# Kernel tuning notes

Hardware: AMD Instinct MI355X
Metric: run time of the kernel (lower is better)

Reference implementation:

```python
import jax, jax.numpy as jnp
import numpy as np

NUM_CIRCLES = 7
B, D_IN, D_HID, D_OUT = 4096, 2048, 3584, 2048  # D_HID % 7 == 0 (7 * 512)


def setup_inputs() -> dict:
    key = jax.random.key(0)
    k1, k2, k3, k4 = jax.random.split(key, 4)
    x = jax.random.normal(k1, (B, D_IN), dtype=jnp.float32)
    # FlowerOfLife: 7 bias-free Linear(D_IN -> D_HID//7) weights, stacked [7, D_HID//7, D_IN]
    W_flower = jax.random.normal(k2, (NUM_CIRCLES, D_HID // NUM_CIRCLES, D_IN), dtype=jnp.float32) / np.sqrt(D_IN).astype(np.float32)
    # Merkaba: two bias-free Linear(D_HID -> D_OUT)
    W_male = jax.random.normal(k3, (D_OUT, D_HID), dtype=jnp.float32) / np.sqrt(D_HID).astype(np.float32)
    W_female = jax.random.normal(k4, (D_OUT, D_HID), dtype=jnp.float32) / np.sqrt(D_HID).astype(np.float32)
    return {"x": x, "W_flower": W_flower, "W_male": W_male, "W_female": W_female}


def reference(x, W_flower, W_male, W_female):
    # --- VesicaPiscisOperation: sacred overlap with the batch-rolled neighbor ---
    x2 = jnp.roll(x, 1, axis=0)
    dist = jnp.linalg.norm(x - x2, axis=1, keepdims=True)          # [B, 1]
    overlap = jax.nn.relu(1.0 - jnp.abs(dist - 1.0))               # [B, 1]
    x_overlap = x * (1.0 + overlap)                                # per-row scaling

    # --- FlowerOfLifeProjection: 7 parallel projections, phase-shift first 2 dims ---
    circ = jnp.einsum('bd,cod->bco', x_overlap, W_flower)          # [B, 7, D_HID//7]
    phases = 2.0 * jnp.pi * jnp.arange(NUM_CIRCLES, dtype=jnp.float32) / NUM_CIRCLES
    phase_shift = jnp.stack([jnp.cos(phases), jnp.sin(phases)], axis=-1)  # [7, 2]
    circ = circ.at[:, :, :2].multiply(phase_shift[None, :, :])
    x_expanded = circ.reshape(x.shape[0], -1)                      # [B, D_HID]

    # --- MerkabaRotation: counter-rotating transforms + sigmoid phase lock ---
    male = x_expanded @ W_male.T                                   # [B, D_OUT]
    female = x_expanded[:, ::-1] @ W_female.T                      # flip(-1) then Linear
    phase_lock = jax.nn.sigmoid(jnp.sum(male * female, axis=-1, keepdims=True))
    return phase_lock * male + (1.0 - phase_lock) * female
```

## Files before the change

kernel.cpp:

```cpp
#include <hip/hip_runtime.h>
#include <hip/hip_bf16.h>
#include <math.h>

#define B_DIM 4096
#define D_IN  2048
#define D_HID 3584
#define D_OUT 2048

typedef __bf16 bf16;
typedef float  floatx4 __attribute__((ext_vector_type(4)));
typedef bf16   bf16x8  __attribute__((ext_vector_type(8)));
typedef bf16   bf16x4  __attribute__((ext_vector_type(4)));

typedef __attribute__((address_space(1))) const void* gptr1;
typedef __attribute__((address_space(3))) void*       lptr3;

__device__ __forceinline__ void load_lds16(const void* g, void* l) {
    __builtin_amdgcn_global_load_lds((gptr1)g, (lptr3)l, 16, 0, 0);
}

struct HL { bf16 h, l; };
__device__ __forceinline__ HL split2(float v) {
    HL r;
    r.h = (bf16)v;
    r.l = (bf16)(v - (float)r.h);
    return r;
}

__global__ __launch_bounds__(256) void vesica_kernel(const float* __restrict__ x,
                                                     bf16* __restrict__ xh,
                                                     bf16* __restrict__ xl) {
    const int b  = blockIdx.x;
    const int bp = (b == 0) ? (B_DIM - 1) : (b - 1);
    const int t  = threadIdx.x;

    const floatx4* xr = (const floatx4*)(x + (size_t)b  * D_IN);
    const floatx4* pr = (const floatx4*)(x + (size_t)bp * D_IN);
    const floatx4 v0 = xr[t * 2], v1 = xr[t * 2 + 1];
    const floatx4 p0 = pr[t * 2], p1 = pr[t * 2 + 1];

    float s = 0.f;
#pragma unroll
    for (int j = 0; j < 4; ++j) {
        const float d0 = v0[j] - p0[j], d1 = v1[j] - p1[j];
        s += d0 * d0 + d1 * d1;
    }
#pragma unroll
    for (int off = 32; off > 0; off >>= 1) s += __shfl_down(s, off, 64);

    __shared__ float red[4];
    const int wave = t >> 6, lane = t & 63;
    if (lane == 0) red[wave] = s;
    __syncthreads();
    const float dist = sqrtf(red[0] + red[1] + red[2] + red[3]);
    const float sc   = 1.f + fmaxf(0.f, 1.f - fabsf(dist - 1.f));

    bf16x8 h, l;
#pragma unroll
    for (int j = 0; j < 4; ++j) {
        const HL a  = split2(v0[j] * sc);
        const HL b2 = split2(v1[j] * sc);
        h[j] = a.h;      l[j] = a.l;
        h[4 + j] = b2.h; l[4 + j] = b2.l;
    }
    ((bf16x8*)(xh + (size_t)b * D_IN))[t] = h;
    ((bf16x8*)(xl + (size_t)b * D_IN))[t] = l;
}

__global__ __launch_bounds__(256) void split_kernel(const float* __restrict__ w,
                                                    bf16* __restrict__ wh,
                                                    bf16* __restrict__ wl) {
    const size_t i = (size_t)blockIdx.x * 256 + threadIdx.x;
    const floatx4 a = ((const floatx4*)w)[i * 2];
    const floatx4 b = ((const floatx4*)w)[i * 2 + 1];
    bf16x8 h, l;
#pragma unroll
    for (int j = 0; j < 4; ++j) {
        const HL u = split2(a[j]);
        const HL v = split2(b[j]);
        h[j] = u.h;     l[j] = u.l;
        h[4 + j] = v.h; l[4 + j] = v.l;
    }
    ((bf16x8*)wh)[i] = h;
    ((bf16x8*)wl)[i] = l;
}

__global__ __launch_bounds__(256) void flipsplit_kernel(const float* __restrict__ w,
                                                        bf16* __restrict__ wh,
                                                        bf16* __restrict__ wl) {
    const int i = blockIdx.x * 256 + threadIdx.x;
    const int o = i / 448;
    const int g = i - o * 448;
    const float* src = w + (size_t)o * 3584 + (size_t)(447 - g) * 8;
    const floatx4 a = ((const floatx4*)src)[0];
    const floatx4 b = ((const floatx4*)src)[1];
    bf16x8 h, l;
#pragma unroll
    for (int j = 0; j < 4; ++j) {
        const HL u = split2(b[3 - j]);
        const HL v = split2(a[3 - j]);
        h[j] = u.h;     l[j] = u.l;
        h[4 + j] = v.h; l[4 + j] = v.l;
    }
    ((bf16x8*)wh)[(size_t)o * 448 + g] = h;
    ((bf16x8*)wl)[(size_t)o * 448 + g] = l;
}

__global__ __launch_bounds__(256) void tsplit_kernel(const float* __restrict__ w,
                                                     bf16* __restrict__ th,
                                                     bf16* __restrict__ tl) {
    __shared__ float tile[64][65];
    const int d0 = blockIdx.x * 64;
    const int h0 = blockIdx.y * 64;
    const int t  = threadIdx.x;
    const int r  = t >> 4;
    const int cg = (t & 15) << 2;

#pragma unroll
    for (int i = 0; i < 4; ++i) {
        const int hr = r + i * 16;
        const floatx4 v = *(const floatx4*)&w[(size_t)(h0 + hr) * 2048 + d0 + cg];
        tile[hr][cg]     = v[0];
        tile[hr][cg + 1] = v[1];
        tile[hr][cg + 2] = v[2];
        tile[hr][cg + 3] = v[3];
    }
    __syncthreads();

    float pm[4];
#pragma unroll
    for (int j = 0; j < 4; ++j) {
        const int h  = h0 + cg + j;
        const int hm = h & 511;
        float p = 1.f;
        if (hm < 2) {
            const float ph = 0.8975979010256552f * (float)(h >> 9);
            p = (hm == 0) ? cosf(ph) : sinf(ph);
        }
        pm[j] = p;
    }

#pragma unroll
    for (int i = 0; i < 4; ++i) {
        const int dr = r + i * 16;
        bf16x4 hh, ll;
#pragma unroll
        for (int j = 0; j < 4; ++j) {
            const HL u = split2(tile[cg + j][dr] * pm[j]);
            hh[j] = u.h;
            ll[j] = u.l;
        }
        const size_t o = (size_t)(d0 + dr) * 3584 + h0 + cg;
        *(bf16x4*)&th[o] = hh;
        *(bf16x4*)&tl[o] = ll;
    }
}

__global__ __launch_bounds__(512, 2) void gemm3_single(const bf16* __restrict__ Ah,
                                                       const bf16* __restrict__ Al,
                                                       const bf16* __restrict__ Bh,
                                                       const bf16* __restrict__ Bl,
                                                       bf16* __restrict__ C0,
                                                       bf16* __restrict__ C1,
                                                       int M, int N, int K) {
    __shared__ bf16 sAh[2][8192], sAl[2][8192];
    __shared__ bf16 sBh[2][4096], sBl[2][4096];

    const int tid  = threadIdx.x;
    const int wave = tid >> 6;
    const int lane = tid & 63;
    const int m0   = blockIdx.y * 256;
    const int n0   = blockIdx.x * 128;
    const int wm   = wave >> 1;
    const int wn   = wave & 1;

    floatx4 acc[4][4];
#pragma unroll
    for (int i = 0; i < 4; ++i)
#pragma unroll
        for (int j = 0; j < 4; ++j) acc[i][j] = (floatx4){0.f, 0.f, 0.f, 0.f};

    const int lr  = lane & 15;
    const int cq  = lane >> 4;
    const int hsw = (lr >> 1) & 7;

    auto stage = [&](int kt, int bsel) {
#pragma unroll
        for (int i = 0; i < 2; ++i) {
            const int q = (i << 9) + tid;
            const int p = q ^ ((q >> 3) & 7);
            const int r = p >> 2, c = p & 3;
            const size_t ga = (size_t)(m0 + r) * K + kt + c * 8;
            load_lds16(&Ah[ga], &sAh[bsel][q << 3]);
            load_lds16(&Al[ga], &sAl[bsel][q << 3]);
        }
        {
            const int q = tid;
            const int p = q ^ ((q >> 3) & 7);
            const int r = p >> 2, c = p & 3;
            const size_t gb = (size_t)(n0 + r) * K + kt + c * 8;
            load_lds16(&Bh[gb], &sBh[bsel][q << 3]);
            load_lds16(&Bl[gb], &sBl[bsel][q << 3]);
        }
    };

    stage(0, 0);
    __syncthreads();

    int buf = 0;
    for (int kt = 0; kt < K; kt += 32) {
        if (kt + 32 < K) stage(kt + 32, buf ^ 1);

        bf16x8 ahf[4], alf[4], bhf[4], blf[4];
#pragma unroll
        for (int mi = 0; mi < 4; ++mi) {
            const int row = wm * 64 + mi * 16 + lr;
            const int off = (((row << 2) + cq) ^ hsw) << 3;
            ahf[mi] = *(const bf16x8*)&sAh[buf][off];
            alf[mi] = *(const bf16x8*)&sAl[buf][off];
        }
#pragma unroll
        for (int ni = 0; ni < 4; ++ni) {
            const int row = wn * 64 + ni * 16 + lr;
            const int off = (((row << 2) + cq) ^ hsw) << 3;
            bhf[ni] = *(const bf16x8*)&sBh[buf][off];
            blf[ni] = *(const bf16x8*)&sBl[buf][off];
        }

#pragma unroll
        for (int mi = 0; mi < 4; ++mi)
#pragma unroll
            for (int ni = 0; ni < 4; ++ni) {
                acc[mi][ni] = __builtin_amdgcn_mfma_f32_16x16x32_bf16(
                    ahf[mi], bhf[ni], acc[mi][ni], 0, 0, 0);
                acc[mi][ni] = __builtin_amdgcn_mfma_f32_16x16x32_bf16(
                    alf[mi], bhf[ni], acc[mi][ni], 0, 0, 0);
                acc[mi][ni] = __builtin_amdgcn_mfma_f32_16x16x32_bf16(
                    ahf[mi], blf[ni], acc[mi][ni], 0, 0, 0);
            }

        __syncthreads();
        buf ^= 1;
    }

    const int rq = (lane >> 4) << 2;
    const int cl = lane & 15;
#pragma unroll
    for (int mi = 0; mi < 4; ++mi) {
#pragma unroll
        for (int ni = 0; ni < 4; ++ni) {
            const int col = n0 + wn * 64 + ni * 16 + cl;
#pragma unroll
            for (int r = 0; r < 4; ++r) {
                const int row = m0 + wm * 64 + mi * 16 + rq + r;
                const size_t idx = (size_t)row * N + col;
                const HL u = split2(acc[mi][ni][r]);
                C0[idx] = u.h;
                C1[idx] = u.l;
            }
        }
    }
}

__global__ __launch_bounds__(512, 2) void gemm3_dual(const bf16* __restrict__ Ah,
                                                     const bf16* __restrict__ Al,
                                                     const bf16* __restrict__ Bmh,
                                                     const bf16* __restrict__ Bml,
                                                     const bf16* __restrict__ Bfh,
                                                     const bf16* __restrict__ Bfl,
                                                     float* __restrict__ Cm,
                                                     float* __restrict__ Cf,
                                                     int M, int N, int K) {
    __shared__ bf16 sAh[2][8192], sAl[2][8192];
    __shared__ bf16 sMh[2][4096], sMl[2][4096];
    __shared__ bf16 sFh[2][4096], sFl[2][4096];

    const int tid  = threadIdx.x;
    const int wave = tid >> 6;
    const int lane = tid & 63;
    const int m0   = blockIdx.y * 256;
    const int n0   = blockIdx.x * 128;
    const int wm   = wave >> 1;
    const int wn   = wave & 1;

    floatx4 am[4][4], af[4][4];
#pragma unroll
    for (int i = 0; i < 4; ++i)
#pragma unroll
        for (int j = 0; j < 4; ++j) {
            am[i][j] = (floatx4){0.f, 0.f, 0.f, 0.f};
            af[i][j] = (floatx4){0.f, 0.f, 0.f, 0.f};
        }

    const int lr  = lane & 15;
    const int cq  = lane >> 4;
    const int hsw = (lr >> 1) & 7;

    auto stage = [&](int kt, int bsel) {
#pragma unroll
        for (int i = 0; i < 2; ++i) {
            const int q = (i << 9) + tid;
            const int p = q ^ ((q >> 3) & 7);
            const int r = p >> 2, c = p & 3;
            const size_t ga = (size_t)(m0 + r) * K + kt + c * 8;
            load_lds16(&Ah[ga], &sAh[bsel][q << 3]);
            load_lds16(&Al[ga], &sAl[bsel][q << 3]);
        }
        {
            const int q = tid;
            const int p = q ^ ((q >> 3) & 7);
            const int r = p >> 2, c = p & 3;
            const size_t gb = (size_t)(n0 + r) * K + kt + c * 8;
            load_lds16(&Bmh[gb], &sMh[bsel][q << 3]);
            load_lds16(&Bml[gb], &sMl[bsel][q << 3]);
            load_lds16(&Bfh[gb], &sFh[bsel][q << 3]);
            load_lds16(&Bfl[gb], &sFl[bsel][q << 3]);
        }
    };

    stage(0, 0);
    __syncthreads();

    int buf = 0;
    for (int kt = 0; kt < K; kt += 32) {
        if (kt + 32 < K) stage(kt + 32, buf ^ 1);

        bf16x8 ahf[4], alf[4];
#pragma unroll
        for (int mi = 0; mi < 4; ++mi) {
            const int row = wm * 64 + mi * 16 + lr;
            const int off = (((row << 2) + cq) ^ hsw) << 3;
            ahf[mi] = *(const bf16x8*)&sAh[buf][off];
            alf[mi] = *(const bf16x8*)&sAl[buf][off];
        }
#pragma unroll
        for (int ni = 0; ni < 4; ++ni) {
            const int row = wn * 64 + ni * 16 + lr;
            const int off = (((row << 2) + cq) ^ hsw) << 3;
            const bf16x8 mh = *(const bf16x8*)&sMh[buf][off];
            const bf16x8 ml = *(const bf16x8*)&sMl[buf][off];
            const bf16x8 fh = *(const bf16x8*)&sFh[buf][off];
            const bf16x8 fl = *(const bf16x8*)&sFl[buf][off];
#pragma unroll
            for (int mi = 0; mi < 4; ++mi) {
                am[mi][ni] = __builtin_amdgcn_mfma_f32_16x16x32_bf16(
                    ahf[mi], mh, am[mi][ni], 0, 0, 0);
                am[mi][ni] = __builtin_amdgcn_mfma_f32_16x16x32_bf16(
                    alf[mi], mh, am[mi][ni], 0, 0, 0);
                am[mi][ni] = __builtin_amdgcn_mfma_f32_16x16x32_bf16(
                    ahf[mi], ml, am[mi][ni], 0, 0, 0);
                af[mi][ni] = __builtin_amdgcn_mfma_f32_16x16x32_bf16(
                    ahf[mi], fh, af[mi][ni], 0, 0, 0);
                af[mi][ni] = __builtin_amdgcn_mfma_f32_16x16x32_bf16(
                    alf[mi], fh, af[mi][ni], 0, 0, 0);
                af[mi][ni] = __builtin_amdgcn_mfma_f32_16x16x32_bf16(
                    ahf[mi], fl, af[mi][ni], 0, 0, 0);
            }
        }

        __syncthreads();
        buf ^= 1;
    }

    const int rq = (lane >> 4) << 2;
    const int cl = lane & 15;
#pragma unroll
    for (int mi = 0; mi < 4; ++mi) {
#pragma unroll
        for (int ni = 0; ni < 4; ++ni) {
            const int col = n0 + wn * 64 + ni * 16 + cl;
#pragma unroll
            for (int r = 0; r < 4; ++r) {
                const int row = m0 + wm * 64 + mi * 16 + rq + r;
                const size_t idx = (size_t)row * N + col;
                Cm[idx] = am[mi][ni][r];
                Cf[idx] = af[mi][ni][r];
            }
        }
    }
}

__global__ __launch_bounds__(256) void combine_kernel(const float* __restrict__ male,
                                                      const float* __restrict__ female,
                                                      float* __restrict__ out) {
    const int b = blockIdx.x;
    const int t = threadIdx.x;

    const floatx4* m4 = (const floatx4*)(male   + (size_t)b * D_OUT);
    const floatx4* f4 = (const floatx4*)(female + (size_t)b * D_OUT);
    const floatx4 mv0 = m4[t * 2], mv1 = m4[t * 2 + 1];
    const floatx4 fv0 = f4[t * 2], fv1 = f4[t * 2 + 1];

    float s = 0.f;
#pragma unroll
    for (int j = 0; j < 4; ++j) s += mv0[j] * fv0[j] + mv1[j] * fv1[j];
#pragma unroll
    for (int off = 32; off > 0; off >>= 1) s += __shfl_down(s, off, 64);

    __shared__ float red[4];
    const int wave = t >> 6, lane = t & 63;
    if (lane == 0) red[wave] = s;
    __syncthreads();
    const float dot = red[0] + red[1] + red[2] + red[3];
    const float pl  = 1.f / (1.f + expf(-dot));

    floatx4 o0, o1;
#pragma unroll
    for (int j = 0; j < 4; ++j) {
        o0[j] = pl * mv0[j] + (1.f - pl) * fv0[j];
        o1[j] = pl * mv1[j] + (1.f - pl) * fv1[j];
    }
    floatx4* o4 = (floatx4*)(out + (size_t)b * D_OUT);
    o4[t * 2]     = o0;
    o4[t * 2 + 1] = o1;
}

extern "C" void kernel_launch(void* const* d_in, const int* in_sizes, int n_in,
                              void* d_out, int out_size, void* d_ws, size_t ws_size,
                              hipStream_t stream) {
    const float* x   = (const float*)d_in[0];
    const float* Wfl = (const float*)d_in[1];
    const float* Wm  = (const float*)d_in[2];
    const float* Wfe = (const float*)d_in[3];
    float* out = (float*)d_out;
    (void)in_sizes; (void)n_in; (void)out_size; (void)ws_size;

    char* ws = (char*)d_ws;
    bf16*  xo_hi   = (bf16*)(ws);
    bf16*  xo_lo   = (bf16*)(ws + 16777216);
    bf16*  Wc_hi   = (bf16*)(ws + 33554432);
    bf16*  Wc_lo   = (bf16*)(ws + 50331648);
    bf16*  WflT_hi = (bf16*)(ws + 67108864);
    bf16*  WflT_lo = (bf16*)(ws + 81788928);
    bf16*  Wcat_hi = (bf16*)(ws + 96468992);
    bf16*  Wcat_lo = (bf16*)(ws + 125829120);
    float* male    = (float*)(ws + 67108864);
    float* female  = (float*)(ws + 100663296);

    vesica_kernel<<<B_DIM, 256, 0, stream>>>(x, xo_hi, xo_lo);

    tsplit_kernel<<<dim3(D_IN / 64, D_HID / 64), 256, 0, stream>>>(Wfl, WflT_hi, WflT_lo);

    split_kernel<<<(D_OUT * D_HID / 8) / 256, 256, 0, stream>>>(Wm, Wcat_hi, Wcat_lo);
    flipsplit_kernel<<<(D_OUT * (D_HID / 8)) / 256, 256, 0, stream>>>(
        Wfe, Wcat_hi + (size_t)D_OUT * D_HID, Wcat_lo + (size_t)D_OUT * D_HID);

    gemm3_single<<<dim3(D_IN / 128, (2 * D_OUT) / 256), 512, 0, stream>>>(
        Wcat_hi, Wcat_lo, WflT_hi, WflT_lo, Wc_hi, Wc_lo,
        2 * D_OUT, D_IN, D_HID);

    gemm3_dual<<<dim3(D_OUT / 128, B_DIM / 256), 512, 0, stream>>>(
        xo_hi, xo_lo,
        Wc_hi, Wc_lo,
        Wc_hi + (size_t)D_OUT * D_IN, Wc_lo + (size_t)D_OUT * D_IN,
        male, female, B_DIM, D_OUT, D_IN);

    combine_kernel<<<B_DIM, 256, 0, stream>>>(male, female, out);
}
```

Baseline: 547.4 us.

## Unify GEMMs into 128x128 templated kernel and split dual GEMM into two launches

Replaces the 256x128-tile single and dual GEMM kernels with one templated 128x128-tile, 256-thread kernel that writes either bf16 hi/lo splits or fp32 output. The dual male/female GEMM becomes two separate launches that each re-read the activation operand. The smaller tile lowers LDS and register use and increases the block count. In exchange, each block reuses less data per tile, the x operand is loaded twice from global memory, and one more kernel is launched.

```diff
diff --git a/kernel.cpp b/kernel.cpp
--- a/kernel.cpp
+++ b/kernel.cpp
@@ -156,23 +156,24 @@
     }
 }
 
-__global__ __launch_bounds__(512, 2) void gemm3_single(const bf16* __restrict__ Ah,
-                                                       const bf16* __restrict__ Al,
-                                                       const bf16* __restrict__ Bh,
-                                                       const bf16* __restrict__ Bl,
-                                                       bf16* __restrict__ C0,
-                                                       bf16* __restrict__ C1,
-                                                       int M, int N, int K) {
-    __shared__ bf16 sAh[2][8192], sAl[2][8192];
+template<int BF16OUT>
+__global__ __launch_bounds__(256, 2) void gemm3_db(const bf16* __restrict__ Ah,
+                                                   const bf16* __restrict__ Al,
+                                                   const bf16* __restrict__ Bh,
+                                                   const bf16* __restrict__ Bl,
+                                                   void* __restrict__ C0p,
+                                                   void* __restrict__ C1p,
+                                                   int M, int N, int K) {
+    __shared__ bf16 sAh[2][4096], sAl[2][4096];
     __shared__ bf16 sBh[2][4096], sBl[2][4096];
 
     const int tid  = threadIdx.x;
     const int wave = tid >> 6;
     const int lane = tid & 63;
-    const int m0   = blockIdx.y * 256;
+    const int m0   = blockIdx.y * 128;
     const int n0   = blockIdx.x * 128;
-    const int wm   = wave >> 1;
-    const int wn   = wave & 1;
+    const int wm   = wave & 1;
+    const int wn   = wave >> 1;
 
     floatx4 acc[4][4];
 #pragma unroll
@@ -187,18 +188,13 @@
     auto stage = [&](int kt, int bsel) {
 #pragma unroll
         for (int i = 0; i < 2; ++i) {
-            const int q = (i << 9) + tid;
+            const int q = (i << 8) + tid;
             const int p = q ^ ((q >> 3) & 7);
             const int r = p >> 2, c = p & 3;
             const size_t ga = (size_t)(m0 + r) * K + kt + c * 8;
+            const size_t gb = (size_t)(n0 + r) * K + kt + c * 8;
             load_lds16(&Ah[ga], &sAh[bsel][q << 3]);
             load_lds16(&Al[ga], &sAl[bsel][q << 3]);
-        }
-        {
-            const int q = tid;
-            const int p = q ^ ((q >> 3) & 7);
-            const int r = p >> 2, c = p & 3;
-            const size_t gb = (size_t)(n0 + r) * K + kt + c * 8;
             load_lds16(&Bh[gb], &sBh[bsel][q << 3]);
             load_lds16(&Bl[gb], &sBl[bsel][q << 3]);
         }
@@ -211,7 +207,7 @@
     for (int kt = 0; kt < K; kt += 32) {
         if (kt + 32 < K) stage(kt + 32, buf ^ 1);
 
-        bf16x8 ahf[4], alf[4], bhf[4], blf[4];
+        bf16x8 ahf[4], alf[4];
 #pragma unroll
         for (int mi = 0; mi < 4; ++mi) {
             const int row = wm * 64 + mi * 16 + lr;
@@ -223,21 +219,18 @@
         for (int ni = 0; ni < 4; ++ni) {
             const int row = wn * 64 + ni * 16 + lr;
             const int off = (((row << 2) + cq) ^ hsw) << 3;
-            bhf[ni] = *(const bf16x8*)&sBh[buf][off];
-            blf[ni] = *(const bf16x8*)&sBl[buf][off];
-        }
-
-#pragma unroll
-        for (int mi = 0; mi < 4; ++mi)
-#pragma unroll
-            for (int ni = 0; ni < 4; ++ni) {
+            const bf16x8 bh = *(const bf16x8*)&sBh[buf][off];
+            const bf16x8 bl = *(const bf16x8*)&sBl[buf][off];
+#pragma unroll
+            for (int mi = 0; mi < 4; ++mi) {
                 acc[mi][ni] = __builtin_amdgcn_mfma_f32_16x16x32_bf16(
-                    ahf[mi], bhf[ni], acc[mi][ni], 0, 0, 0);
+                    ahf[mi], bh, acc[mi][ni], 0, 0, 0);
                 acc[mi][ni] = __builtin_amdgcn_mfma_f32_16x16x32_bf16(
-                    alf[mi], bhf[ni], acc[mi][ni], 0, 0, 0);
+                    alf[mi], bh, acc[mi][ni], 0, 0, 0);
                 acc[mi][ni] = __builtin_amdgcn_mfma_f32_16x16x32_bf16(
-                    ahf[mi], blf[ni], acc[mi][ni], 0, 0, 0);
+                    ahf[mi], bl, acc[mi][ni], 0, 0, 0);
             }
+        }
 
         __syncthreads();
         buf ^= 1;
@@ -254,127 +247,13 @@
             for (int r = 0; r < 4; ++r) {
                 const int row = m0 + wm * 64 + mi * 16 + rq + r;
                 const size_t idx = (size_t)row * N + col;
-                const HL u = split2(acc[mi][ni][r]);
-                C0[idx] = u.h;
-                C1[idx] = u.l;
-            }
-        }
-    }
-}
-
-__global__ __launch_bounds__(512, 2) void gemm3_dual(const bf16* __restrict__ Ah,
-                                                     const bf16* __restrict__ Al,
-                                                     const bf16* __restrict__ Bmh,
-                                                     const bf16* __restrict__ Bml,
-                                                     const bf16* __restrict__ Bfh,
-                                                     const bf16* __restrict__ Bfl,
-                                                     float* __restrict__ Cm,
-                                                     float* __restrict__ Cf,
-                                                     int M, int N, int K) {
-    __shared__ bf16 sAh[2][8192], sAl[2][8192];
-    __shared__ bf16 sMh[2][4096], sMl[2][4096];
-    __shared__ bf16 sFh[2][4096], sFl[2][4096];
-
-    const int tid  = threadIdx.x;
-    const int wave = tid >> 6;
-    const int lane = tid & 63;
-    const int m0   = blockIdx.y * 256;
-    const int n0   = blockIdx.x * 128;
-    const int wm   = wave >> 1;
-    const int wn   = wave & 1;
-
-    floatx4 am[4][4], af[4][4];
-#pragma unroll
-    for (int i = 0; i < 4; ++i)
-#pragma unroll
-        for (int j = 0; j < 4; ++j) {
-            am[i][j] = (floatx4){0.f, 0.f, 0.f, 0.f};
-            af[i][j] = (floatx4){0.f, 0.f, 0.f, 0.f};
-        }
-
-    const int lr  = lane & 15;
-    const int cq  = lane >> 4;
-    const int hsw = (lr >> 1) & 7;
-
-    auto stage = [&](int kt, int bsel) {
-#pragma unroll
-        for (int i = 0; i < 2; ++i) {
-            const int q = (i << 9) + tid;
-            const int p = q ^ ((q >> 3) & 7);
-            const int r = p >> 2, c = p & 3;
-            const size_t ga = (size_t)(m0 + r) * K + kt + c * 8;
-            load_lds16(&Ah[ga], &sAh[bsel][q << 3]);
-            load_lds16(&Al[ga], &sAl[bsel][q << 3]);
-        }
-        {
-            const int q = tid;
-            const int p = q ^ ((q >> 3) & 7);
-            const int r = p >> 2, c = p & 3;
-            const size_t gb = (size_t)(n0 + r) * K + kt + c * 8;
-            load_lds16(&Bmh[gb], &sMh[bsel][q << 3]);
-            load_lds16(&Bml[gb], &sMl[bsel][q << 3]);
-            load_lds16(&Bfh[gb], &sFh[bsel][q << 3]);
-            load_lds16(&Bfl[gb], &sFl[bsel][q << 3]);
-        }
-    };
-
-    stage(0, 0);
-    __syncthreads();
-
-    int buf = 0;
-    for (int kt = 0; kt < K; kt += 32) {
-        if (kt + 32 < K) stage(kt + 32, buf ^ 1);
-
-        bf16x8 ahf[4], alf[4];
-#pragma unroll
-        for (int mi = 0; mi < 4; ++mi) {
-            const int row = wm * 64 + mi * 16 + lr;
-            const int off = (((row << 2) + cq) ^ hsw) << 3;
-            ahf[mi] = *(const bf16x8*)&sAh[buf][off];
-            alf[mi] = *(const bf16x8*)&sAl[buf][off];
-        }
-#pragma unroll
-        for (int ni = 0; ni < 4; ++ni) {
-            const int row = wn * 64 + ni * 16 + lr;
-            const int off = (((row << 2) + cq) ^ hsw) << 3;
-            const bf16x8 mh = *(const bf16x8*)&sMh[buf][off];
-            const bf16x8 ml = *(const bf16x8*)&sMl[buf][off];
-            const bf16x8 fh = *(const bf16x8*)&sFh[buf][off];
-            const bf16x8 fl = *(const bf16x8*)&sFl[buf][off];
-#pragma unroll
-            for (int mi = 0; mi < 4; ++mi) {
-                am[mi][ni] = __builtin_amdgcn_mfma_f32_16x16x32_bf16(
-                    ahf[mi], mh, am[mi][ni], 0, 0, 0);
-                am[mi][ni] = __builtin_amdgcn_mfma_f32_16x16x32_bf16(
-                    alf[mi], mh, am[mi][ni], 0, 0, 0);
-                am[mi][ni] = __builtin_amdgcn_mfma_f32_16x16x32_bf16(
-                    ahf[mi], ml, am[mi][ni], 0, 0, 0);
-                af[mi][ni] = __builtin_amdgcn_mfma_f32_16x16x32_bf16(
-                    ahf[mi], fh, af[mi][ni], 0, 0, 0);
-                af[mi][ni] = __builtin_amdgcn_mfma_f32_16x16x32_bf16(
-                    alf[mi], fh, af[mi][ni], 0, 0, 0);
-                af[mi][ni] = __builtin_amdgcn_mfma_f32_16x16x32_bf16(
-                    ahf[mi], fl, af[mi][ni], 0, 0, 0);
-            }
-        }
-
-        __syncthreads();
-        buf ^= 1;
-    }
-
-    const int rq = (lane >> 4) << 2;
-    const int cl = lane & 15;
-#pragma unroll
-    for (int mi = 0; mi < 4; ++mi) {
-#pragma unroll
-        for (int ni = 0; ni < 4; ++ni) {
-            const int col = n0 + wn * 64 + ni * 16 + cl;
-#pragma unroll
-            for (int r = 0; r < 4; ++r) {
-                const int row = m0 + wm * 64 + mi * 16 + rq + r;
-                const size_t idx = (size_t)row * N + col;
-                Cm[idx] = am[mi][ni][r];
-                Cf[idx] = af[mi][ni][r];
+                if constexpr (BF16OUT) {
+                    const HL u = split2(acc[mi][ni][r]);
+                    ((bf16*)C0p)[idx] = u.h;
+                    ((bf16*)C1p)[idx] = u.l;
+                } else {
+                    ((float*)C0p)[idx] = acc[mi][ni][r];
+                }
             }
         }
     }
@@ -445,15 +324,18 @@
     flipsplit_kernel<<<(D_OUT * (D_HID / 8)) / 256, 256, 0, stream>>>(
         Wfe, Wcat_hi + (size_t)D_OUT * D_HID, Wcat_lo + (size_t)D_OUT * D_HID);
 
-    gemm3_single<<<dim3(D_IN / 128, (2 * D_OUT) / 256), 512, 0, stream>>>(
+    gemm3_db<1><<<dim3(D_IN / 128, (2 * D_OUT) / 128), 256, 0, stream>>>(
         Wcat_hi, Wcat_lo, WflT_hi, WflT_lo, Wc_hi, Wc_lo,
         2 * D_OUT, D_IN, D_HID);
 
-    gemm3_dual<<<dim3(D_OUT / 128, B_DIM / 256), 512, 0, stream>>>(
+    gemm3_db<0><<<dim3(D_OUT / 128, B_DIM / 128), 256, 0, stream>>>(
+        xo_hi, xo_lo, Wc_hi, Wc_lo, male, nullptr,
+        B_DIM, D_OUT, D_IN);
+
+    gemm3_db<0><<<dim3(D_OUT / 128, B_DIM / 128), 256, 0, stream>>>(
         xo_hi, xo_lo,
-        Wc_hi, Wc_lo,
         Wc_hi + (size_t)D_OUT * D_IN, Wc_lo + (size_t)D_OUT * D_IN,
-        male, female, B_DIM, D_OUT, D_IN);
+        female, nullptr, B_DIM, D_OUT, D_IN);
 
     combine_kernel<<<B_DIM, 256, 0, stream>>>(male, female, out);
 }
```

Result: no change. 536.9 us (-1.9%).
